# Kernel tuning notes

Hardware: AMD Instinct MI355X
Metric: run time of the kernel (lower is better)

The kernel has to match this reference:

```python
import jax, jax.numpy as jnp
import numpy as np

N, D, K = 500_000, 64, 512


def setup_inputs() -> dict:
    key = jax.random.key(0)
    kx, kc = jax.random.split(key)
    x = jax.random.normal(kx, (N, D), dtype=jnp.float32)
    centroids = jax.random.normal(kc, (K, D), dtype=jnp.float32)
    return {"x": x, "centroids": centroids}


def reference(x, centroids):
    x2 = jnp.sum(x * x, axis=1, keepdims=True)            # [N, 1]
    c2 = jnp.sum(centroids * centroids, axis=1)           # [K]
    d2 = x2 + c2[None, :] - 2.0 * jnp.einsum('nd,kd->nk', x, centroids)
    d2 = jnp.maximum(d2, 0.0)
    # sqrt is monotonic so argmin over d2 == argmin over cdist
    label = jnp.argmin(d2, axis=1)                        # [N] int
    return label
```

## Files before the change

kernel.cpp:

```cpp
#include <hip/hip_runtime.h>

#define DIM 64
#define KC 512
#define BLK 256
#define BLKP 256
#define RSB 256
#define PT 2
#define CG 64
#define NT (CG / 16)
#define NGRP (KC / CG)
#define MARGINH 5e-4f
#define LIST_CAP 500000

typedef _Float16 half8   __attribute__((ext_vector_type(8)));
typedef float    floatx4 __attribute__((ext_vector_type(4)));

__device__ __forceinline__ void async_cp16(_Float16* lds_base, const _Float16* g_lane) {
    __builtin_amdgcn_global_load_lds(
        (const __attribute__((address_space(1))) unsigned int*)(g_lane),
        (__attribute__((address_space(3))) unsigned int*)(lds_base),
        16, 0, 0);
}

__global__ __launch_bounds__(BLKP) void kmeans_prep(
    const float* __restrict__ c, _Float16* __restrict__ frH,
    _Float16* __restrict__ frL, float* __restrict__ g_sc2,
    unsigned* __restrict__ rs_count)
{
    const int b = blockIdx.x;
    if (b < 128) {
        const int e  = b * BLKP + threadIdx.x;
        const int cr = e >> 6, d = e & 63;
        const int T  = cr >> 4, ni = cr & 15;
        const int ch = d >> 5, q = (d >> 3) & 3, j = d & 7;
        const int pos = ((T * 2 + ch) * 64 + (q * 16 + ni)) * 8 + j;
        const float f = c[e];
        const _Float16 h = (_Float16)f;
        frH[pos] = h;
        frL[pos] = (_Float16)((f - (float)h) * 2048.0f);
    } else {
        if (b == 128 && threadIdx.x == 0) *rs_count = 0u;
        const int k = (b - 128) * BLKP + threadIdx.x;
        const float* crow = c + (long)k * DIM;
        float s0 = 0.f, s1 = 0.f, s2 = 0.f, s3 = 0.f;
        #pragma unroll
        for (int d = 0; d < DIM; d += 4) {
            s0 = fmaf(crow[d + 0], crow[d + 0], s0);
            s1 = fmaf(crow[d + 1], crow[d + 1], s1);
            s2 = fmaf(crow[d + 2], crow[d + 2], s2);
            s3 = fmaf(crow[d + 3], crow[d + 3], s3);
        }
        g_sc2[k] = (s0 + s1) + (s2 + s3);
    }
}

__global__ __launch_bounds__(BLK)
__attribute__((amdgpu_waves_per_eu(2)))
void kmeans_mfma(const float* __restrict__ x,
                 const _Float16* __restrict__ frH, const _Float16* __restrict__ frL,
                 const float* __restrict__ g_sc2, int* __restrict__ out,
                 unsigned* __restrict__ rs_count, int* __restrict__ rs_list, int n)
{
    __shared__ _Float16 shH[NT * 2 * 64 * 8];
    __shared__ _Float16 shL[NT * 2 * 64 * 8];
    __shared__ float    s_sc2[KC];

    const int tid  = threadIdx.x;
    const int wave = tid >> 6;
    const int lane = tid & 63;
    const int nidx = lane & 15;
    const int quad = lane >> 4;

    const long jobBase = ((long)blockIdx.x * 4 + wave) * (PT * 16);

    half8 ah[PT][2], al[PT][2];
    #pragma unroll
    for (int pt = 0; pt < PT; ++pt) {
        long row = jobBase + pt * 16 + nidx;
        if (row > (long)n - 1) row = (long)n - 1;
        #pragma unroll
        for (int ch = 0; ch < 2; ++ch) {
            const float* xp = x + row * DIM + ch * 32 + quad * 8;
            float4 v0 = *(const float4*)xp;
            float4 v1 = *(const float4*)(xp + 4);
            float fs[8] = {v0.x, v0.y, v0.z, v0.w, v1.x, v1.y, v1.z, v1.w};
            #pragma unroll
            for (int j = 0; j < 8; ++j) {
                _Float16 h = (_Float16)fs[j];
                ah[pt][ch][j] = h;
                al[pt][ch][j] = (_Float16)((fs[j] - (float)h) * 2048.0f);
            }
        }
    }

    float best[PT][4], sec[PT][4];
    int   bidx[PT][4];
    #pragma unroll
    for (int pt = 0; pt < PT; ++pt)
        #pragma unroll
        for (int r = 0; r < 4; ++r) {
            best[pt][r] = -3.402823466e38f;
            sec[pt][r]  = -3.402823466e38f;
            bidx[pt][r] = 0;
        }

    for (int g = 0; g < NGRP; ++g) {
        if (g) __syncthreads();

        {
            const _Float16* srcH = frH + (long)g * (NT * 2 * 64 * 8);
            const _Float16* srcL = frL + (long)g * (NT * 2 * 64 * 8);
            #pragma unroll
            for (int ii = 0; ii < 2; ++ii) {
                const int chunk = (ii * 4 + wave) * 64;
                async_cp16(shH + (long)chunk * 8, srcH + (long)(chunk + lane) * 8);
                async_cp16(shL + (long)chunk * 8, srcL + (long)(chunk + lane) * 8);
            }
        }
        if (g == 0) {
            for (int k2 = tid; k2 < KC; k2 += BLK) s_sc2[k2] = g_sc2[k2];
        }
        __syncthreads();

        #pragma unroll 2
        for (int t = 0; t < NT; ++t) {
            const half8 bh0 = *(const half8*)&shH[((t * 2 + 0) * 64 + lane) * 8];
            const half8 bh1 = *(const half8*)&shH[((t * 2 + 1) * 64 + lane) * 8];
            const half8 bl0 = *(const half8*)&shL[((t * 2 + 0) * 64 + lane) * 8];
            const half8 bl1 = *(const half8*)&shL[((t * 2 + 1) * 64 + lane) * 8];
            const float negh = -0.5f * s_sc2[g * CG + t * 16 + nidx];
            const int   kidx = g * CG + t * 16 + nidx;
            #pragma unroll
            for (int pt = 0; pt < PT; ++pt) {
                floatx4 am = {negh, negh, negh, negh};
                floatx4 ac = {0.f, 0.f, 0.f, 0.f};
                am = __builtin_amdgcn_mfma_f32_16x16x32_f16(ah[pt][0], bh0, am, 0, 0, 0);
                am = __builtin_amdgcn_mfma_f32_16x16x32_f16(ah[pt][1], bh1, am, 0, 0, 0);
                ac = __builtin_amdgcn_mfma_f32_16x16x32_f16(ah[pt][0], bl0, ac, 0, 0, 0);
                ac = __builtin_amdgcn_mfma_f32_16x16x32_f16(ah[pt][1], bl1, ac, 0, 0, 0);
                ac = __builtin_amdgcn_mfma_f32_16x16x32_f16(al[pt][0], bh0, ac, 0, 0, 0);
                ac = __builtin_amdgcn_mfma_f32_16x16x32_f16(al[pt][1], bh1, ac, 0, 0, 0);
                const floatx4 vv = am + ac * 4.8828125e-4f;
                #pragma unroll
                for (int r = 0; r < 4; ++r) {
                    const bool gt = vv[r] > best[pt][r];
                    sec[pt][r]  = __builtin_amdgcn_fmed3f(sec[pt][r], vv[r], best[pt][r]);
                    best[pt][r] = fmaxf(best[pt][r], vv[r]);
                    bidx[pt][r] = gt ? kidx : bidx[pt][r];
                }
            }
        }
    }

    #pragma unroll
    for (int off = 1; off < 16; off <<= 1) {
        #pragma unroll
        for (int pt = 0; pt < PT; ++pt)
            #pragma unroll
            for (int r = 0; r < 4; ++r) {
                const float ob = __shfl_xor(best[pt][r], off, 64);
                const int   oi = __shfl_xor(bidx[pt][r], off, 64);
                const float os = __shfl_xor(sec[pt][r],  off, 64);
                const bool take = (ob > best[pt][r]) ||
                                  (ob == best[pt][r] && oi < bidx[pt][r]);
                const float loser = take ? best[pt][r] : ob;
                sec[pt][r]  = fmaxf(fmaxf(sec[pt][r], os), loser);
                best[pt][r] = take ? ob : best[pt][r];
                bidx[pt][r] = take ? oi : bidx[pt][r];
            }
    }

    const int pt_w = nidx >> 2;
    const int r_w  = nidx & 3;
    float b = 0.f, s = 0.f; int bi = 0;
    #pragma unroll
    for (int pt = 0; pt < PT; ++pt)
        #pragma unroll
        for (int r = 0; r < 4; ++r) {
            const bool m = (pt == pt_w) && (r == r_w);
            b  = m ? best[pt][r] : b;
            s  = m ? sec[pt][r]  : s;
            bi = m ? bidx[pt][r] : bi;
        }
    const long p = jobBase + (long)pt_w * 16 + quad * 4 + r_w;

    if (nidx < 8 && p < n) {
        out[p] = bi;
        if (!(b - s > MARGINH)) {
            const unsigned idx = atomicAdd(rs_count, 1u);
            if (idx < LIST_CAP) rs_list[idx] = (int)p;
        }
    }
}

__global__ __launch_bounds__(RSB) void kmeans_rescan(
    const float* __restrict__ x, const float* __restrict__ c,
    const float* __restrict__ g_sc2, const unsigned* __restrict__ rs_count,
    const int* __restrict__ rs_list, int* __restrict__ out)
{
    __shared__ float4 ct4[16 * 513];
    __shared__ float  s_c2[KC];

    const int tid = threadIdx.x;
    for (int e = tid; e < KC * 16; e += RSB) {
        const int k = e >> 4, d4 = e & 15;
        ct4[d4 * 513 + k] = *(const float4*)(c + (long)k * DIM + d4 * 4);
    }
    for (int k = tid; k < KC; k += RSB) s_c2[k] = g_sc2[k];
    __syncthreads();

    const int lane  = tid & 63;
    const int gwave = blockIdx.x * (RSB / 64) + (tid >> 6);
    const int nwave = gridDim.x * (RSB / 64);
    unsigned cnt = *rs_count;
    if (cnt > LIST_CAP) cnt = LIST_CAP;

    for (unsigned j = gwave; j < cnt; j += nwave) {
        const int p = rs_list[j];
        const float* xrow = x + (long)p * DIM;

        float x20 = 0.f, x21 = 0.f, x22 = 0.f, x23 = 0.f;
        #pragma unroll
        for (int d = 0; d < DIM; d += 4) {
            x20 = fmaf(xrow[d + 0], xrow[d + 0], x20);
            x21 = fmaf(xrow[d + 1], xrow[d + 1], x21);
            x22 = fmaf(xrow[d + 2], xrow[d + 2], x22);
            x23 = fmaf(xrow[d + 3], xrow[d + 3], x23);
        }
        const float x2 = (x20 + x21) + (x22 + x23);

        float bb = 3.402823466e38f; int bbi = 0x7fffffff;
        #pragma unroll
        for (int kk = 0; kk < 8; ++kk) {
            const int k = kk * 64 + lane;
            float d0 = 0.f, d1 = 0.f, d2a = 0.f, d3 = 0.f;
            #pragma unroll
            for (int d4 = 0; d4 < 16; ++d4) {
                const float4 q = ct4[d4 * 513 + k];
                d0  = fmaf(q.x, xrow[4 * d4 + 0], d0);
                d1  = fmaf(q.y, xrow[4 * d4 + 1], d1);
                d2a = fmaf(q.z, xrow[4 * d4 + 2], d2a);
                d3  = fmaf(q.w, xrow[4 * d4 + 3], d3);
            }
            const float dot = (d0 + d1) + (d2a + d3);
            float d2v = (x2 + s_c2[k]) - 2.0f * dot;
            d2v = fmaxf(d2v, 0.0f);
            const bool l2 = (d2v < bb) || (d2v == bb && k < bbi);
            bb  = l2 ? d2v : bb;
            bbi = l2 ? k   : bbi;
        }
        #pragma unroll
        for (int off = 1; off < 64; off <<= 1) {
            const float ob = __shfl_xor(bb, off, 64);
            const int   oi = __shfl_xor(bbi, off, 64);
            const bool take = (ob < bb) || (ob == bb && oi < bbi);
            bb  = take ? ob : bb;
            bbi = take ? oi : bbi;
        }
        if (lane == 0) out[p] = bbi;
    }
}

extern "C" void kernel_launch(void* const* d_in, const int* in_sizes, int n_in,
                              void* d_out, int out_size, void* d_ws, size_t ws_size,
                              hipStream_t stream) {
    const float* x = (const float*)d_in[0];
    const float* c = (const float*)d_in[1];
    int* out = (int*)d_out;
    const int n = in_sizes[0] / DIM;

    _Float16* frH   = (_Float16*)d_ws;
    _Float16* frL   = frH + (KC * DIM);
    float*    gsc2  = (float*)(frL + (KC * DIM));
    unsigned* cnt   = (unsigned*)(gsc2 + KC);
    int*      rlist = (int*)(cnt + 4);

    kmeans_prep<<<130, BLKP, 0, stream>>>(c, frH, frL, gsc2, cnt);

    const int jobs   = (n + PT * 16 - 1) / (PT * 16);
    const int blocks = (jobs + 3) / 4;
    kmeans_mfma<<<blocks, BLK, 0, stream>>>(x, frH, frL, gsc2, out, cnt, rlist, n);

    kmeans_rescan<<<256, RSB, 0, stream>>>(x, c, gsc2, cnt, rlist, out);
}
```

Before: 291.8 us.

## Drop fp16 split-precision correction, use error-bound margin, double-buffer centroids

Removes the low-order fp16 correction terms, so each tile issues 2 MFMAs instead of 6 and stages half as much centroid data into LDS. To stay exact, the fixed rescan margin becomes a per-row error bound that scales with sqrt(||x||^2 * max||c||^2). Rows whose top-two gap falls inside that bound go to the fp32 rescan kernel. Centroid staging is also double-buffered so the next group's async copy overlaps compute, and one barrier per group is dropped. The wider margin may send many more rows to rescan, which could offset the MFMA savings.

```diff
diff --git a/kernel.cpp b/kernel.cpp
--- a/kernel.cpp
+++ b/kernel.cpp
@@ -9,8 +9,10 @@
 #define CG 64
 #define NT (CG / 16)
 #define NGRP (KC / CG)
-#define MARGINH 5e-4f
 #define LIST_CAP 500000
+
+#define THR_A 2.0e-3f
+#define THR_B 2.5e-3f
 
 typedef _Float16 half8   __attribute__((ext_vector_type(8)));
 typedef float    floatx4 __attribute__((ext_vector_type(4)));
@@ -24,8 +26,7 @@
 
 __global__ __launch_bounds__(BLKP) void kmeans_prep(
     const float* __restrict__ c, _Float16* __restrict__ frH,
-    _Float16* __restrict__ frL, float* __restrict__ g_sc2,
-    unsigned* __restrict__ rs_count)
+    float* __restrict__ g_sc2, unsigned* __restrict__ rs_count)
 {
     const int b = blockIdx.x;
     if (b < 128) {
@@ -34,10 +35,7 @@
         const int T  = cr >> 4, ni = cr & 15;
         const int ch = d >> 5, q = (d >> 3) & 3, j = d & 7;
         const int pos = ((T * 2 + ch) * 64 + (q * 16 + ni)) * 8 + j;
-        const float f = c[e];
-        const _Float16 h = (_Float16)f;
-        frH[pos] = h;
-        frL[pos] = (_Float16)((f - (float)h) * 2048.0f);
+        frH[pos] = (_Float16)c[e];
     } else {
         if (b == 128 && threadIdx.x == 0) *rs_count = 0u;
         const int k = (b - 128) * BLKP + threadIdx.x;
@@ -57,12 +55,11 @@
 __global__ __launch_bounds__(BLK)
 __attribute__((amdgpu_waves_per_eu(2)))
 void kmeans_mfma(const float* __restrict__ x,
-                 const _Float16* __restrict__ frH, const _Float16* __restrict__ frL,
+                 const _Float16* __restrict__ frH,
                  const float* __restrict__ g_sc2, int* __restrict__ out,
                  unsigned* __restrict__ rs_count, int* __restrict__ rs_list, int n)
 {
-    __shared__ _Float16 shH[NT * 2 * 64 * 8];
-    __shared__ _Float16 shL[NT * 2 * 64 * 8];
+    __shared__ _Float16 shH[2][NT * 2 * 64 * 8];
     __shared__ float    s_sc2[KC];
 
     const int tid  = threadIdx.x;
@@ -73,11 +70,25 @@
 
     const long jobBase = ((long)blockIdx.x * 4 + wave) * (PT * 16);
 
-    half8 ah[PT][2], al[PT][2];
+    auto stage = [&](int gg, int buf) {
+        const _Float16* srcH = frH + (long)gg * (NT * 2 * 64 * 8);
+        #pragma unroll
+        for (int ii = 0; ii < 2; ++ii) {
+            const int chunk = (ii * 4 + wave) * 64;
+            async_cp16(&shH[buf][(long)chunk * 8], srcH + (long)(chunk + lane) * 8);
+        }
+    };
+
+    stage(0, 0);
+    for (int k2 = tid; k2 < KC; k2 += BLK) s_sc2[k2] = g_sc2[k2];
+
+    half8 ah[PT][2];
+    float x2v[PT];
     #pragma unroll
     for (int pt = 0; pt < PT; ++pt) {
         long row = jobBase + pt * 16 + nidx;
         if (row > (long)n - 1) row = (long)n - 1;
+        float x2p = 0.f;
         #pragma unroll
         for (int ch = 0; ch < 2; ++ch) {
             const float* xp = x + row * DIM + ch * 32 + quad * 8;
@@ -86,11 +97,13 @@
             float fs[8] = {v0.x, v0.y, v0.z, v0.w, v1.x, v1.y, v1.z, v1.w};
             #pragma unroll
             for (int j = 0; j < 8; ++j) {
-                _Float16 h = (_Float16)fs[j];
-                ah[pt][ch][j] = h;
-                al[pt][ch][j] = (_Float16)((fs[j] - (float)h) * 2048.0f);
-            }
-        }
+                ah[pt][ch][j] = (_Float16)fs[j];
+                x2p = fmaf(fs[j], fs[j], x2p);
+            }
+        }
+        x2p += __shfl_xor(x2p, 16, 64);
+        x2p += __shfl_xor(x2p, 32, 64);
+        x2v[pt] = x2p;
     }
 
     float best[PT][4], sec[PT][4];
@@ -104,52 +117,33 @@
             bidx[pt][r] = 0;
         }
 
+    __syncthreads();
+
     for (int g = 0; g < NGRP; ++g) {
-        if (g) __syncthreads();
-
-        {
-            const _Float16* srcH = frH + (long)g * (NT * 2 * 64 * 8);
-            const _Float16* srcL = frL + (long)g * (NT * 2 * 64 * 8);
-            #pragma unroll
-            for (int ii = 0; ii < 2; ++ii) {
-                const int chunk = (ii * 4 + wave) * 64;
-                async_cp16(shH + (long)chunk * 8, srcH + (long)(chunk + lane) * 8);
-                async_cp16(shL + (long)chunk * 8, srcL + (long)(chunk + lane) * 8);
-            }
-        }
-        if (g == 0) {
-            for (int k2 = tid; k2 < KC; k2 += BLK) s_sc2[k2] = g_sc2[k2];
-        }
-        __syncthreads();
-
-        #pragma unroll 2
+        const int cur = g & 1;
+        if (g + 1 < NGRP) stage(g + 1, cur ^ 1);
+
+        #pragma unroll
         for (int t = 0; t < NT; ++t) {
-            const half8 bh0 = *(const half8*)&shH[((t * 2 + 0) * 64 + lane) * 8];
-            const half8 bh1 = *(const half8*)&shH[((t * 2 + 1) * 64 + lane) * 8];
-            const half8 bl0 = *(const half8*)&shL[((t * 2 + 0) * 64 + lane) * 8];
-            const half8 bl1 = *(const half8*)&shL[((t * 2 + 1) * 64 + lane) * 8];
-            const float negh = -0.5f * s_sc2[g * CG + t * 16 + nidx];
+            const half8 bh0 = *(const half8*)&shH[cur][((t * 2 + 0) * 64 + lane) * 8];
+            const half8 bh1 = *(const half8*)&shH[cur][((t * 2 + 1) * 64 + lane) * 8];
             const int   kidx = g * CG + t * 16 + nidx;
+            const float negh = -0.5f * s_sc2[kidx];
             #pragma unroll
             for (int pt = 0; pt < PT; ++pt) {
                 floatx4 am = {negh, negh, negh, negh};
-                floatx4 ac = {0.f, 0.f, 0.f, 0.f};
                 am = __builtin_amdgcn_mfma_f32_16x16x32_f16(ah[pt][0], bh0, am, 0, 0, 0);
                 am = __builtin_amdgcn_mfma_f32_16x16x32_f16(ah[pt][1], bh1, am, 0, 0, 0);
-                ac = __builtin_amdgcn_mfma_f32_16x16x32_f16(ah[pt][0], bl0, ac, 0, 0, 0);
-                ac = __builtin_amdgcn_mfma_f32_16x16x32_f16(ah[pt][1], bl1, ac, 0, 0, 0);
-                ac = __builtin_amdgcn_mfma_f32_16x16x32_f16(al[pt][0], bh0, ac, 0, 0, 0);
-                ac = __builtin_amdgcn_mfma_f32_16x16x32_f16(al[pt][1], bh1, ac, 0, 0, 0);
-                const floatx4 vv = am + ac * 4.8828125e-4f;
                 #pragma unroll
                 for (int r = 0; r < 4; ++r) {
-                    const bool gt = vv[r] > best[pt][r];
-                    sec[pt][r]  = __builtin_amdgcn_fmed3f(sec[pt][r], vv[r], best[pt][r]);
-                    best[pt][r] = fmaxf(best[pt][r], vv[r]);
+                    const bool gt = am[r] > best[pt][r];
+                    sec[pt][r]  = __builtin_amdgcn_fmed3f(sec[pt][r], am[r], best[pt][r]);
+                    best[pt][r] = fmaxf(best[pt][r], am[r]);
                     bidx[pt][r] = gt ? kidx : bidx[pt][r];
                 }
             }
         }
+        if (g + 1 < NGRP) __syncthreads();
     }
 
     #pragma unroll
@@ -170,6 +164,12 @@
             }
     }
 
+    float c2m = s_sc2[lane];
+    #pragma unroll
+    for (int k2 = 64; k2 < KC; k2 += 64) c2m = fmaxf(c2m, s_sc2[lane + k2]);
+    #pragma unroll
+    for (int off = 1; off < 64; off <<= 1) c2m = fmaxf(c2m, __shfl_xor(c2m, off, 64));
+
     const int pt_w = nidx >> 2;
     const int r_w  = nidx & 3;
     float b = 0.f, s = 0.f; int bi = 0;
@@ -182,11 +182,17 @@
             s  = m ? sec[pt][r]  : s;
             bi = m ? bidx[pt][r] : bi;
         }
+    const int   srcl = quad * 4 + r_w;
+    const float xxa  = __shfl(x2v[0], srcl, 64);
+    const float xxb  = __shfl(x2v[1], srcl, 64);
+    const float xx   = (pt_w == 0) ? xxa : xxb;
+    const float thr  = fmaf(THR_A, sqrtf(xx * c2m), THR_B);
+
     const long p = jobBase + (long)pt_w * 16 + quad * 4 + r_w;
 
     if (nidx < 8 && p < n) {
         out[p] = bi;
-        if (!(b - s > MARGINH)) {
+        if (!(b - s > thr)) {
             const unsigned idx = atomicAdd(rs_count, 1u);
             if (idx < LIST_CAP) rs_list[idx] = (int)p;
         }
@@ -270,16 +276,15 @@
     const int n = in_sizes[0] / DIM;
 
     _Float16* frH   = (_Float16*)d_ws;
-    _Float16* frL   = frH + (KC * DIM);
-    float*    gsc2  = (float*)(frL + (KC * DIM));
+    float*    gsc2  = (float*)(frH + (KC * DIM));
     unsigned* cnt   = (unsigned*)(gsc2 + KC);
     int*      rlist = (int*)(cnt + 4);
 
-    kmeans_prep<<<130, BLKP, 0, stream>>>(c, frH, frL, gsc2, cnt);
+    kmeans_prep<<<130, BLKP, 0, stream>>>(c, frH, gsc2, cnt);
 
     const int jobs   = (n + PT * 16 - 1) / (PT * 16);
     const int blocks = (jobs + 3) / 4;
-    kmeans_mfma<<<blocks, BLK, 0, stream>>>(x, frH, frL, gsc2, out, cnt, rlist, n);
+    kmeans_mfma<<<blocks, BLK, 0, stream>>>(x, frH, gsc2, out, cnt, rlist, n);
 
     kmeans_rescan<<<256, RSB, 0, stream>>>(x, c, gsc2, cnt, rlist, out);
 }
```

New measurement: 591.4 us. +102.6%, slower.
